# Kernel tuning notes

Measured on AMD Instinct MI355X. Metric: run time of the kernel, lower is better.

The kernel has to match this reference:

```python
import jax, jax.numpy as jnp
import numpy as np

B, S, D, H = 4, 2048, 1024, 16
DK = D // H
NEG = -1e9  # stand-in for -inf; keeps softmax grads NaN-free, same math after softmax


def setup_inputs() -> dict:
    key = jax.random.key(0)
    ks = jax.random.split(key, 8)
    scale = 0.02
    return {
        "q": jax.random.normal(ks[0], (B, S, D), jnp.float32),
        "k": jax.random.normal(ks[1], (B, S, D), jnp.float32),
        "v": jax.random.normal(ks[2], (B, S, D), jnp.float32),
        "mask": jnp.ones((B, S), jnp.int32),
        "Wq": jax.random.normal(ks[3], (D, D), jnp.float32) * scale,
        "bq": jnp.zeros((D,), jnp.float32),
        "Wk": jax.random.normal(ks[4], (D, D), jnp.float32) * scale,
        "bk": jnp.zeros((D,), jnp.float32),
        "Wv": jax.random.normal(ks[5], (D, D), jnp.float32) * scale,
        "bv": jnp.zeros((D,), jnp.float32),
        "Wp": jax.random.normal(ks[6], (D, D), jnp.float32) * scale,
        "bp": jnp.zeros((D,), jnp.float32),
    }


def reference(q, k, v, mask, Wq, bq, Wk, bk, Wv, bv, Wp, bp):
    # torch.nn.Linear: y = x @ W.T + b
    Q = q @ Wq.T + bq  # [B,S,D]
    K = k @ Wk.T + bk
    V = v @ Wv.T + bv
    # split heads -> [B,H,S,dk]
    Q = Q.reshape(B, S, H, DK).transpose(0, 2, 1, 3)
    K = K.reshape(B, S, H, DK).transpose(0, 2, 1, 3)
    V = V.reshape(B, S, H, DK).transpose(0, 2, 1, 3)
    Sc = jnp.einsum("bhqd,bhkd->bhqk", Q, K) / jnp.sqrt(jnp.float32(DK))
    # padding mask: [B,1,1,Sk]
    Sc = jnp.where(mask[:, None, None, :] == 0, NEG, Sc)
    # causal mask (tril), as in the registered buffer
    causal = jnp.tril(jnp.ones((S, S), jnp.bool_))
    Sc = jnp.where(causal, Sc, NEG)
    A = jax.nn.softmax(Sc, axis=-1)  # attn_drop with p=0 is identity
    x = jnp.einsum("bhqk,bhkd->bhqd", A, V)
    x = x.transpose(0, 2, 1, 3).reshape(B, S, D)
    return x @ Wp.T + bp
```

## Files before the change

### kernel.cpp

```cpp
#include <hip/hip_runtime.h>
#include <stdint.h>


#define SZB (8192u * 1024u * 2u)
#define WSZ (1024u * 1024u * 2u)

typedef __attribute__((ext_vector_type(8))) short  short8;
typedef __attribute__((ext_vector_type(4))) float  f32x4;

#define MFMA16(a, b, c) __builtin_amdgcn_mfma_f32_16x16x32_bf16(a, b, c, 0, 0, 0)

__device__ __forceinline__ ushort f2bf(float f) {
  uint32_t u = __float_as_uint(f);
  u += 0x7FFF + ((u >> 16) & 1);
  return (ushort)(u >> 16);
}
__device__ __forceinline__ short8 cvt8(float4 a, float4 b) {
  short8 r;
  r[0] = (short)f2bf(a.x); r[1] = (short)f2bf(a.y);
  r[2] = (short)f2bf(a.z); r[3] = (short)f2bf(a.w);
  r[4] = (short)f2bf(b.x); r[5] = (short)f2bf(b.y);
  r[6] = (short)f2bf(b.z); r[7] = (short)f2bf(b.w);
  return r;
}
__device__ __forceinline__ void gl_lds16(const ushort* g, ushort* l) {
  __builtin_amdgcn_global_load_lds(
      (__attribute__((address_space(1))) void*)g,
      (__attribute__((address_space(3))) void*)l, 16, 0, 0);
}

__global__ __launch_bounds__(256) void cvt_w(
    const float* __restrict__ Wq, const float* __restrict__ Wk,
    const float* __restrict__ Wv, const float* __restrict__ Wp,
    ushort* __restrict__ Wqb, ushort* __restrict__ Wkb,
    ushort* __restrict__ Wvb, ushort* __restrict__ Wpb) {
  const int z = blockIdx.y;
  const float* s = (z == 0) ? Wq : (z == 1) ? Wk : (z == 2) ? Wv : Wp;
  ushort* d = (z == 0) ? Wqb : (z == 1) ? Wkb : (z == 2) ? Wvb : Wpb;
  const size_t i = (size_t)(blockIdx.x * 256 + threadIdx.x) * 8;
  *(short8*)&d[i] = cvt8(*(const float4*)&s[i], *(const float4*)&s[i + 4]);
}

__global__ __launch_bounds__(256) void cvt_in(
    const float* __restrict__ q, const float* __restrict__ k,
    const float* __restrict__ v,
    ushort* __restrict__ qb2, ushort* __restrict__ kb2,
    ushort* __restrict__ vb2) {
  const int z = blockIdx.y;
  const float* s = (z == 0) ? q : (z == 1) ? k : v;
  ushort* d = (z == 0) ? qb2 : (z == 1) ? kb2 : vb2;
  const size_t i = (size_t)(blockIdx.x * 256 + threadIdx.x) * 8;
  *(short8*)&d[i] = cvt8(*(const float4*)&s[i], *(const float4*)&s[i + 4]);
}

__device__ __forceinline__ void gemm_core_mixed(
    const float* __restrict__ A, const ushort* __restrict__ Wb,
    ushort* As, ushort* Bs, int m0, int n0, f32x4 acc[4][4]) {
  const int tid  = threadIdx.x;
  const int w    = tid >> 6;
  const int lane = tid & 63;
  const int quad = lane >> 4;
  const int l16  = lane & 15;
  const int wm   = (w >> 1) * 64;
  const int wn   = (w & 1) * 64;
  const int r0   = tid >> 2;
  const int r1   = r0 + 64;
  const int c0   = (tid & 3) * 8;

  const ushort* Wg = Wb + (size_t)(n0 + w * 32 + (lane >> 2)) * 1024 + (lane & 3) * 8;
  const float*  Ag0 = A + (size_t)(m0 + r0) * 1024 + c0;
  const float*  Ag1 = A + (size_t)(m0 + r1) * 1024 + c0;

  float4 p0a = *(const float4*)(Ag0), p0b = *(const float4*)(Ag0 + 4);
  float4 p1a = *(const float4*)(Ag1), p1b = *(const float4*)(Ag1 + 4);

  for (int kt = 0; kt < 32; ++kt) {
    const int ko = kt * 32;
    __syncthreads();
    *(short8*)&As[r0 * 32 + c0] = cvt8(p0a, p0b);
    *(short8*)&As[r1 * 32 + c0] = cvt8(p1a, p1b);
    gl_lds16(Wg + ko,         &Bs[(w * 32) * 32]);
    gl_lds16(Wg + 16384 + ko, &Bs[(w * 32 + 16) * 32]);
    __syncthreads();
    if (kt < 31) {
      const int kn = ko + 32;
      p0a = *(const float4*)(Ag0 + kn); p0b = *(const float4*)(Ag0 + kn + 4);
      p1a = *(const float4*)(Ag1 + kn); p1b = *(const float4*)(Ag1 + kn + 4);
    }
    short8 af[4], bfr[4];
#pragma unroll
    for (int i = 0; i < 4; ++i)
      af[i] = *(const short8*)&As[(wm + i * 16 + l16) * 32 + quad * 8];
#pragma unroll
    for (int i = 0; i < 4; ++i)
      bfr[i] = *(const short8*)&Bs[(wn + i * 16 + l16) * 32 + quad * 8];
#pragma unroll
    for (int i = 0; i < 4; ++i)
#pragma unroll
      for (int j = 0; j < 4; ++j)
        acc[i][j] = MFMA16(af[i], bfr[j], acc[i][j]);
  }
}

__device__ __forceinline__ void gemm_core_bf(
    const ushort* __restrict__ A, const ushort* __restrict__ Wb,
    ushort* As, ushort* Bs, int m0, int n0, f32x4 acc[4][4]) {
  const int tid  = threadIdx.x;
  const int w    = tid >> 6;
  const int lane = tid & 63;
  const int quad = lane >> 4;
  const int l16  = lane & 15;
  const int wm   = (w >> 1) * 64;
  const int wn   = (w & 1) * 64;

  const ushort* Ag = A + (size_t)(m0 + w * 32 + (lane >> 2)) * 1024 + (lane & 3) * 8;
  const ushort* Wg = Wb + (size_t)(n0 + w * 32 + (lane >> 2)) * 1024 + (lane & 3) * 8;

  for (int kt = 0; kt < 32; ++kt) {
    const int ko = kt * 32;
    gl_lds16(Ag + ko,         &As[(w * 32) * 32]);
    gl_lds16(Ag + 16384 + ko, &As[(w * 32 + 16) * 32]);
    gl_lds16(Wg + ko,         &Bs[(w * 32) * 32]);
    gl_lds16(Wg + 16384 + ko, &Bs[(w * 32 + 16) * 32]);
    __syncthreads();

    short8 af[4], bfr[4];
#pragma unroll
    for (int i = 0; i < 4; ++i)
      af[i] = *(const short8*)&As[(wm + i * 16 + l16) * 32 + quad * 8];
#pragma unroll
    for (int i = 0; i < 4; ++i)
      bfr[i] = *(const short8*)&Bs[(wn + i * 16 + l16) * 32 + quad * 8];
#pragma unroll
    for (int i = 0; i < 4; ++i)
#pragma unroll
      for (int j = 0; j < 4; ++j)
        acc[i][j] = MFMA16(af[i], bfr[j], acc[i][j]);
    __syncthreads();
  }
}

__global__ __launch_bounds__(256) void gemm_qkv(
    const ushort* __restrict__ qb2, const ushort* __restrict__ kb2,
    const ushort* __restrict__ vb2, const float* __restrict__ vin, int v_bf,
    const ushort* __restrict__ Wqb, const ushort* __restrict__ Wkb, const ushort* __restrict__ Wvb,
    const float* __restrict__ bq, const float* __restrict__ bk, const float* __restrict__ bv,
    ushort* __restrict__ Qb, ushort* __restrict__ Kb, ushort* __restrict__ Vt) {
  __shared__ ushort As[128 * 32];
  __shared__ ushort Bs[128 * 32];

  const int z = blockIdx.z;
  const ushort* W    = (z == 0) ? Wqb : (z == 1) ? Wkb : Wvb;
  const float*  bias = (z == 0) ? bq  : (z == 1) ? bk  : bv;

  const int m0 = blockIdx.x * 128;
  const int n0 = blockIdx.y * 128;

  f32x4 acc[4][4] = {};
  if (z == 2 && !v_bf) {
    gemm_core_mixed(vin, W, As, Bs, m0, n0, acc);
  } else {
    const ushort* A = (z == 0) ? qb2 : (z == 1) ? kb2 : vb2;
    gemm_core_bf(A, W, As, Bs, m0, n0, acc);
  }

  const int tid  = threadIdx.x;
  const int w    = tid >> 6;
  const int lane = tid & 63;
  const int quad = lane >> 4;
  const int l16  = lane & 15;
  const int wm   = (w >> 1) * 64;
  const int wn   = (w & 1) * 64;

  float bvv[4];
#pragma unroll
  for (int j = 0; j < 4; ++j) bvv[j] = bias[n0 + wn + j * 16 + l16];

  if (z < 2) {
    ushort* Out = (z == 0) ? Qb : Kb;
    const float sc = (z == 0) ? 0.1803368801f : 1.0f;
#pragma unroll
    for (int i = 0; i < 4; ++i) {
      const int m = m0 + wm + i * 16 + quad * 4;
#pragma unroll
      for (int j = 0; j < 4; ++j) {
        const int n = n0 + wn + j * 16 + l16;
#pragma unroll
        for (int r = 0; r < 4; ++r)
          Out[(size_t)(m + r) * 1024 + n] = f2bf((acc[i][j][r] + bvv[j]) * sc);
      }
    }
  } else {
#pragma unroll
    for (int i = 0; i < 4; ++i) {
      const int mrow = m0 + wm + i * 16 + quad * 4;
      const int bb   = mrow >> 11;
      const int s0   = mrow & 2047;
#pragma unroll
      for (int j = 0; j < 4; ++j) {
        const int n = n0 + wn + j * 16 + l16;
        ushort4 pk;
        pk.x = f2bf(acc[i][j][0] + bvv[j]);
        pk.y = f2bf(acc[i][j][1] + bvv[j]);
        pk.z = f2bf(acc[i][j][2] + bvv[j]);
        pk.w = f2bf(acc[i][j][3] + bvv[j]);
        *(ushort4*)&Vt[(size_t)((bb * 16 + (n >> 6)) * 64 + (n & 63)) * 2048 + s0] = pk;
      }
    }
  }
}

__global__ __launch_bounds__(256, 4) void attn(
    ushort* __restrict__ Qb, const ushort* __restrict__ Kb,
    const ushort* __restrict__ Vt, const int* __restrict__ mask) {
  __shared__ ushort Ks[64 * 68];
  __shared__ ushort Vts[64 * 68];
  __shared__ ushort Ps[4][16 * 68];

  const int bh = blockIdx.y;
  const int b = bh >> 4, h = bh & 15;
  const int tid = threadIdx.x, w = tid >> 6, lane = tid & 63;
  const int quad = lane >> 4, l16 = lane & 15;

  short8 kst[2], vst[2];
  int pmn[4];

  auto ld_tile = [&](int k0) {
#pragma unroll
    for (int i = 0; i < 2; ++i) {
      const int c = tid + 256 * i;
      kst[i] = *(const short8*)&Kb[(size_t)(b * 2048 + k0 + (c >> 3)) * 1024 +
                                   h * 64 + (c & 7) * 8];
      vst[i] = *(const short8*)&Vt[(size_t)(bh * 64 + (c >> 3)) * 2048 +
                                   k0 + (c & 7) * 8];
    }
#pragma unroll
    for (int nj = 0; nj < 4; ++nj) pmn[nj] = mask[b * 2048 + k0 + nj * 16 + l16];
  };

#pragma unroll 1
  for (int seg = 0; seg < 2; ++seg) {
    const int qt = seg ? (31 - (int)blockIdx.x) : (int)blockIdx.x;
    const int q0 = qt * 64;

    const size_t qoff = (size_t)(b * 2048 + q0 + w * 16 + l16) * 1024 + h * 64 + quad * 8;
    const short8 qf0 = *(const short8*)&Qb[qoff];
    const short8 qf1 = *(const short8*)&Qb[qoff + 32];

    f32x4 oacc[4] = {};
    float lsum[4] = {0.f, 0.f, 0.f, 0.f};

    ld_tile(0);

    for (int kt = 0; kt <= qt; ++kt) {
      __syncthreads();
#pragma unroll
      for (int i = 0; i < 2; ++i) {
        const int c = tid + 256 * i;
        *(short8*)&Ks[(c >> 3) * 68 + (c & 7) * 8]  = kst[i];
        *(short8*)&Vts[(c >> 3) * 68 + (c & 7) * 8] = vst[i];
      }
      int pmc[4];
#pragma unroll
      for (int nj = 0; nj < 4; ++nj) pmc[nj] = pmn[nj];
      __syncthreads();

      if (kt < qt) ld_tile((kt + 1) * 64);

      f32x4 sc[4];
#pragma unroll
      for (int nj = 0; nj < 4; ++nj) {
        f32x4 z4 = {0.f, 0.f, 0.f, 0.f};
        const short8 kf0 = *(const short8*)&Ks[(nj * 16 + l16) * 68 + quad * 8];
        const short8 kf1 = *(const short8*)&Ks[(nj * 16 + l16) * 68 + 32 + quad * 8];
        z4 = MFMA16(qf0, kf0, z4);
        z4 = MFMA16(qf1, kf1, z4);
        sc[nj] = z4;
      }

      if (kt < qt) {
#pragma unroll
        for (int nj = 0; nj < 4; ++nj)
#pragma unroll
          for (int r = 0; r < 4; ++r) {
            const float e = (pmc[nj] != 0) ? sc[nj][r] : -1e5f;
            const float p = __builtin_amdgcn_exp2f(e);
            lsum[r] += p;
            Ps[w][(quad * 4 + r) * 68 + nj * 16 + l16] = f2bf(p);
          }
      } else {
        const int k0 = kt * 64;
#pragma unroll
        for (int nj = 0; nj < 4; ++nj) {
          const int key = k0 + nj * 16 + l16;
#pragma unroll
          for (int r = 0; r < 4; ++r) {
            const int qr = q0 + w * 16 + quad * 4 + r;
            const bool ok = (pmc[nj] != 0) && (key <= qr);
            const float e = ok ? sc[nj][r] : -1e5f;
            const float p = __builtin_amdgcn_exp2f(e);
            lsum[r] += p;
            Ps[w][(quad * 4 + r) * 68 + nj * 16 + l16] = f2bf(p);
          }
        }
      }

#pragma unroll
      for (int ks = 0; ks < 2; ++ks) {
        const short8 pf = *(const short8*)&Ps[w][l16 * 68 + ks * 32 + quad * 8];
#pragma unroll
        for (int nb = 0; nb < 4; ++nb) {
          const short8 vf = *(const short8*)&Vts[(nb * 16 + l16) * 68 + ks * 32 + quad * 8];
          oacc[nb] = MFMA16(pf, vf, oacc[nb]);
        }
      }
    }

#pragma unroll
    for (int r = 0; r < 4; ++r) {
      float v = lsum[r];
      v += __shfl_xor(v, 1);
      v += __shfl_xor(v, 2);
      v += __shfl_xor(v, 4);
      v += __shfl_xor(v, 8);
      lsum[r] = 1.0f / v;
    }
#pragma unroll
    for (int nb = 0; nb < 4; ++nb)
#pragma unroll
      for (int r = 0; r < 4; ++r) {
        const int q = q0 + w * 16 + quad * 4 + r;
        Qb[(size_t)(b * 2048 + q) * 1024 + h * 64 + nb * 16 + l16] =
            f2bf(oacc[nb][r] * lsum[r]);
      }
  }
}

__global__ __launch_bounds__(256) void gemm_proj(
    const ushort* __restrict__ Xin, const ushort* __restrict__ Wpb,
    const float* __restrict__ bp, float* __restrict__ Out) {
  __shared__ ushort As[128 * 32];
  __shared__ ushort Bs[128 * 32];

  const int m0 = blockIdx.x * 128;
  const int n0 = blockIdx.y * 128;

  f32x4 acc[4][4] = {};
  gemm_core_bf(Xin, Wpb, As, Bs, m0, n0, acc);

  const int tid  = threadIdx.x;
  const int w    = tid >> 6;
  const int lane = tid & 63;
  const int quad = lane >> 4;
  const int l16  = lane & 15;
  const int wm   = (w >> 1) * 64;
  const int wn   = (w & 1) * 64;

  float bvv[4];
#pragma unroll
  for (int j = 0; j < 4; ++j) bvv[j] = bp[n0 + wn + j * 16 + l16];

#pragma unroll
  for (int i = 0; i < 4; ++i) {
    const int m = m0 + wm + i * 16 + quad * 4;
#pragma unroll
    for (int j = 0; j < 4; ++j) {
      const int n = n0 + wn + j * 16 + l16;
#pragma unroll
      for (int r = 0; r < 4; ++r)
        Out[(size_t)(m + r) * 1024 + n] = acc[i][j][r] + bvv[j];
    }
  }
}

extern "C" void kernel_launch(void* const* d_in, const int* in_sizes, int n_in,
                              void* d_out, int out_size, void* d_ws, size_t ws_size,
                              hipStream_t stream) {
  const float* q    = (const float*)d_in[0];
  const float* k    = (const float*)d_in[1];
  const float* v    = (const float*)d_in[2];
  const int*   mask = (const int*)d_in[3];
  const float* Wq   = (const float*)d_in[4];
  const float* bq   = (const float*)d_in[5];
  const float* Wk   = (const float*)d_in[6];
  const float* bk   = (const float*)d_in[7];
  const float* Wv   = (const float*)d_in[8];
  const float* bv   = (const float*)d_in[9];
  const float* Wp   = (const float*)d_in[10];
  const float* bp   = (const float*)d_in[11];
  float* out = (float*)d_out;

  char* ws = (char*)d_ws;
  ushort* Qb  = (ushort*)(ws);
  ushort* Kb  = (ushort*)(ws + (size_t)SZB);
  ushort* Vt  = (ushort*)(ws + (size_t)2 * SZB);
  ushort* Wqb = (ushort*)(ws + (size_t)3 * SZB);
  ushort* Wkb = (ushort*)(ws + (size_t)3 * SZB + WSZ);
  ushort* Wvb = (ushort*)(ws + (size_t)3 * SZB + 2 * WSZ);
  ushort* Wpb = (ushort*)(ws + (size_t)3 * SZB + 3 * WSZ);

  ushort* qb2 = (ushort*)out;
  ushort* kb2 = (ushort*)((char*)out + (size_t)SZB);
  const size_t need_v = (size_t)3 * SZB + 4 * WSZ + SZB;
  const int v_bf = (ws_size >= need_v) ? 1 : 0;
  ushort* vb2 = v_bf ? (ushort*)(ws + (size_t)3 * SZB + 4 * WSZ) : nullptr;

  dim3 blk(256);
  cvt_w<<<dim3(512, 4), blk, 0, stream>>>(Wq, Wk, Wv, Wp, Wqb, Wkb, Wvb, Wpb);
  cvt_in<<<dim3(4096, 2 + v_bf), blk, 0, stream>>>(q, k, v, qb2, kb2, vb2);
  gemm_qkv<<<dim3(64, 8, 3), blk, 0, stream>>>(qb2, kb2, vb2, v, v_bf,
                                               Wqb, Wkb, Wvb, bq, bk, bv,
                                               Qb, Kb, Vt);
  attn<<<dim3(16, 64), blk, 0, stream>>>(Qb, Kb, Vt, mask);
  gemm_proj<<<dim3(64, 8), blk, 0, stream>>>(Qb, Wpb, bp, out);
}
```

Before: 352.4 us.

## Replace projection GEMM core with triple-buffered 512-thread swizzled-LDS pipeline

Rewrites the QKV and output projection GEMMs around a new core that uses 512-thread blocks with 256x128 tiles, a K-step of 64, and a three-slot LDS ring. Global-to-LDS loads are issued two stages ahead using vmcnt waits and a single barrier per step. Reads are XOR-swizzled to avoid bank conflicts, and MFMA issue priority is raised with setprio. The mixed fp32-input V path moves into a separate fallback kernel. The aim is to hide memory latency and cut sync overhead, at the cost of much more LDS per block (144 KB), which limits occupancy.

```diff
diff --git a/kernel.cpp b/kernel.cpp
--- a/kernel.cpp
+++ b/kernel.cpp
@@ -4,6 +4,8 @@
 
 #define SZB (8192u * 1024u * 2u)
 #define WSZ (1024u * 1024u * 2u)
+#define NKT 16
+#define SLOT 24576
 
 typedef __attribute__((ext_vector_type(8))) short  short8;
 typedef __attribute__((ext_vector_type(4))) float  f32x4;
@@ -53,9 +55,195 @@
   *(short8*)&d[i] = cvt8(*(const float4*)&s[i], *(const float4*)&s[i + 4]);
 }
 
-__device__ __forceinline__ void gemm_core_mixed(
-    const float* __restrict__ A, const ushort* __restrict__ Wb,
-    ushort* As, ushort* Bs, int m0, int n0, f32x4 acc[4][4]) {
+__device__ __forceinline__ void core8p(
+    const ushort* __restrict__ A, const ushort* __restrict__ Wb,
+    ushort* lds, int m0, int n0, f32x4 acc[4][4]) {
+  const int tid  = threadIdx.x;
+  const int w    = tid >> 6;
+  const int lane = tid & 63;
+  const int quad = lane >> 4;
+  const int l16  = lane & 15;
+  const int wm   = (w >> 1) * 64;
+  const int wn   = (w & 1) * 64;
+
+  const ushort* asrc[4];
+  const ushort* bsrc[2];
+#pragma unroll
+  for (int i = 0; i < 4; ++i) {
+    const int c = tid + 512 * i;
+    asrc[i] = A + (size_t)(m0 + (c >> 3)) * 1024 + ((c & 7) ^ ((c >> 3) & 7)) * 8;
+  }
+#pragma unroll
+  for (int i = 0; i < 2; ++i) {
+    const int c = tid + 512 * i;
+    bsrc[i] = Wb + (size_t)(n0 + (c >> 3)) * 1024 + ((c & 7) ^ ((c >> 3) & 7)) * 8;
+  }
+
+  auto stage = [&](int j, int s) {
+    ushort* base = lds + s * SLOT + w * 512;
+#pragma unroll
+    for (int i = 0; i < 4; ++i)
+      gl_lds16(asrc[i] + j * 64, base + i * 4096);
+#pragma unroll
+    for (int i = 0; i < 2; ++i)
+      gl_lds16(bsrc[i] + j * 64, base + 16384 + i * 4096);
+  };
+
+  const int rsw = (l16 & 7) * 8;
+  auto compute = [&](int s) {
+    const ushort* pA = lds + s * SLOT;
+    const ushort* pB = pA + 16384;
+    short8 a[4][2], b[4][2];
+#pragma unroll
+    for (int f = 0; f < 4; ++f)
+#pragma unroll
+      for (int ks = 0; ks < 2; ++ks) {
+        a[f][ks] = *(const short8*)&pA[(wm + f * 16 + l16) * 64 +
+                                       ((ks * 32 + quad * 8) ^ rsw)];
+        b[f][ks] = *(const short8*)&pB[(wn + f * 16 + l16) * 64 +
+                                       ((ks * 32 + quad * 8) ^ rsw)];
+      }
+    __builtin_amdgcn_s_setprio(1);
+#pragma unroll
+    for (int i = 0; i < 4; ++i)
+#pragma unroll
+      for (int j2 = 0; j2 < 4; ++j2) {
+        acc[i][j2] = MFMA16(a[i][0], b[j2][0], acc[i][j2]);
+        acc[i][j2] = MFMA16(a[i][1], b[j2][1], acc[i][j2]);
+      }
+    __builtin_amdgcn_s_setprio(0);
+  };
+
+  stage(0, 0);
+  stage(1, 1);
+  int s = 0;
+#pragma unroll 1
+  for (int j = 0; j < NKT - 1; ++j) {
+    asm volatile("s_waitcnt vmcnt(6)" ::: "memory");
+    __builtin_amdgcn_s_barrier();
+    __builtin_amdgcn_sched_barrier(0);
+    if (j < NKT - 2) {
+      int s2 = s + 2; if (s2 >= 3) s2 -= 3;
+      stage(j + 2, s2);
+    }
+    compute(s);
+    if (++s == 3) s = 0;
+  }
+  asm volatile("s_waitcnt vmcnt(0)" ::: "memory");
+  __builtin_amdgcn_s_barrier();
+  __builtin_amdgcn_sched_barrier(0);
+  compute(s);
+}
+
+__global__ __launch_bounds__(512, 2) void gemm_qkv8(
+    const ushort* __restrict__ qb2, const ushort* __restrict__ kb2,
+    const ushort* __restrict__ vb2,
+    const ushort* __restrict__ Wqb, const ushort* __restrict__ Wkb,
+    const ushort* __restrict__ Wvb,
+    const float* __restrict__ bq, const float* __restrict__ bk,
+    const float* __restrict__ bv,
+    ushort* __restrict__ Qb, ushort* __restrict__ Kb, ushort* __restrict__ Vt) {
+  __shared__ ushort lds[3 * SLOT];
+
+  const int z = blockIdx.z;
+  const ushort* A    = (z == 0) ? qb2 : (z == 1) ? kb2 : vb2;
+  const ushort* W    = (z == 0) ? Wqb : (z == 1) ? Wkb : Wvb;
+  const float*  bias = (z == 0) ? bq  : (z == 1) ? bk  : bv;
+
+  const int m0 = blockIdx.x * 256;
+  const int n0 = blockIdx.y * 128;
+
+  f32x4 acc[4][4] = {};
+  core8p(A, W, lds, m0, n0, acc);
+
+  const int tid  = threadIdx.x;
+  const int w    = tid >> 6;
+  const int lane = tid & 63;
+  const int quad = lane >> 4;
+  const int l16  = lane & 15;
+  const int wm   = (w >> 1) * 64;
+  const int wn   = (w & 1) * 64;
+
+  float bvv[4];
+#pragma unroll
+  for (int j = 0; j < 4; ++j) bvv[j] = bias[n0 + wn + j * 16 + l16];
+
+  if (z < 2) {
+    ushort* Out = (z == 0) ? Qb : Kb;
+    const float sc = (z == 0) ? 0.1803368801f : 1.0f;
+#pragma unroll
+    for (int i = 0; i < 4; ++i) {
+      const int m = m0 + wm + i * 16 + quad * 4;
+#pragma unroll
+      for (int j = 0; j < 4; ++j) {
+        const int n = n0 + wn + j * 16 + l16;
+#pragma unroll
+        for (int r = 0; r < 4; ++r)
+          Out[(size_t)(m + r) * 1024 + n] = f2bf((acc[i][j][r] + bvv[j]) * sc);
+      }
+    }
+  } else {
+#pragma unroll
+    for (int i = 0; i < 4; ++i) {
+      const int mrow = m0 + wm + i * 16 + quad * 4;
+      const int bb   = mrow >> 11;
+      const int s0   = mrow & 2047;
+#pragma unroll
+      for (int j = 0; j < 4; ++j) {
+        const int n = n0 + wn + j * 16 + l16;
+        ushort4 pk;
+        pk.x = f2bf(acc[i][j][0] + bvv[j]);
+        pk.y = f2bf(acc[i][j][1] + bvv[j]);
+        pk.z = f2bf(acc[i][j][2] + bvv[j]);
+        pk.w = f2bf(acc[i][j][3] + bvv[j]);
+        *(ushort4*)&Vt[(size_t)((bb * 16 + (n >> 6)) * 64 + (n & 63)) * 2048 + s0] = pk;
+      }
+    }
+  }
+}
+
+__global__ __launch_bounds__(512, 2) void gemm_proj8(
+    const ushort* __restrict__ Xin, const ushort* __restrict__ Wpb,
+    const float* __restrict__ bp, float* __restrict__ Out) {
+  __shared__ ushort lds[3 * SLOT];
+
+  const int m0 = blockIdx.x * 256;
+  const int n0 = blockIdx.y * 128;
+
+  f32x4 acc[4][4] = {};
+  core8p(Xin, Wpb, lds, m0, n0, acc);
+
+  const int tid  = threadIdx.x;
+  const int w    = tid >> 6;
+  const int lane = tid & 63;
+  const int quad = lane >> 4;
+  const int l16  = lane & 15;
+  const int wm   = (w >> 1) * 64;
+  const int wn   = (w & 1) * 64;
+
+  float bvv[4];
+#pragma unroll
+  for (int j = 0; j < 4; ++j) bvv[j] = bp[n0 + wn + j * 16 + l16];
+
+#pragma unroll
+  for (int i = 0; i < 4; ++i) {
+    const int m = m0 + wm + i * 16 + quad * 4;
+#pragma unroll
+    for (int j = 0; j < 4; ++j) {
+      const int n = n0 + wn + j * 16 + l16;
+#pragma unroll
+      for (int r = 0; r < 4; ++r)
+        Out[(size_t)(m + r) * 1024 + n] = acc[i][j][r] + bvv[j];
+    }
+  }
+}
+
+__global__ __launch_bounds__(256) void gemm_v_fb(
+    const float* __restrict__ vin, const ushort* __restrict__ Wvb,
+    const float* __restrict__ bv, ushort* __restrict__ Vt) {
+  __shared__ ushort As[128 * 32];
+  __shared__ ushort Bs[128 * 32];
+
   const int tid  = threadIdx.x;
   const int w    = tid >> 6;
   const int lane = tid & 63;
@@ -67,9 +255,13 @@
   const int r1   = r0 + 64;
   const int c0   = (tid & 3) * 8;
 
-  const ushort* Wg = Wb + (size_t)(n0 + w * 32 + (lane >> 2)) * 1024 + (lane & 3) * 8;
-  const float*  Ag0 = A + (size_t)(m0 + r0) * 1024 + c0;
-  const float*  Ag1 = A + (size_t)(m0 + r1) * 1024 + c0;
+  const int m0 = blockIdx.x * 128;
+  const int n0 = blockIdx.y * 128;
+
+  f32x4 acc[4][4] = {};
+  const ushort* Wg = Wvb + (size_t)(n0 + w * 32 + (lane >> 2)) * 1024 + (lane & 3) * 8;
+  const float*  Ag0 = vin + (size_t)(m0 + r0) * 1024 + c0;
+  const float*  Ag1 = vin + (size_t)(m0 + r1) * 1024 + c0;
 
   float4 p0a = *(const float4*)(Ag0), p0b = *(const float4*)(Ag0 + 4);
   float4 p1a = *(const float4*)(Ag1), p1b = *(const float4*)(Ag1 + 4);
@@ -100,112 +292,24 @@
       for (int j = 0; j < 4; ++j)
         acc[i][j] = MFMA16(af[i], bfr[j], acc[i][j]);
   }
-}
-
-__device__ __forceinline__ void gemm_core_bf(
-    const ushort* __restrict__ A, const ushort* __restrict__ Wb,
-    ushort* As, ushort* Bs, int m0, int n0, f32x4 acc[4][4]) {
-  const int tid  = threadIdx.x;
-  const int w    = tid >> 6;
-  const int lane = tid & 63;
-  const int quad = lane >> 4;
-  const int l16  = lane & 15;
-  const int wm   = (w >> 1) * 64;
-  const int wn   = (w & 1) * 64;
-
-  const ushort* Ag = A + (size_t)(m0 + w * 32 + (lane >> 2)) * 1024 + (lane & 3) * 8;
-  const ushort* Wg = Wb + (size_t)(n0 + w * 32 + (lane >> 2)) * 1024 + (lane & 3) * 8;
-
-  for (int kt = 0; kt < 32; ++kt) {
-    const int ko = kt * 32;
-    gl_lds16(Ag + ko,         &As[(w * 32) * 32]);
-    gl_lds16(Ag + 16384 + ko, &As[(w * 32 + 16) * 32]);
-    gl_lds16(Wg + ko,         &Bs[(w * 32) * 32]);
-    gl_lds16(Wg + 16384 + ko, &Bs[(w * 32 + 16) * 32]);
-    __syncthreads();
-
-    short8 af[4], bfr[4];
-#pragma unroll
-    for (int i = 0; i < 4; ++i)
-      af[i] = *(const short8*)&As[(wm + i * 16 + l16) * 32 + quad * 8];
-#pragma unroll
-    for (int i = 0; i < 4; ++i)
-      bfr[i] = *(const short8*)&Bs[(wn + i * 16 + l16) * 32 + quad * 8];
-#pragma unroll
-    for (int i = 0; i < 4; ++i)
-#pragma unroll
-      for (int j = 0; j < 4; ++j)
-        acc[i][j] = MFMA16(af[i], bfr[j], acc[i][j]);
-    __syncthreads();
-  }
-}
-
-__global__ __launch_bounds__(256) void gemm_qkv(
-    const ushort* __restrict__ qb2, const ushort* __restrict__ kb2,
-    const ushort* __restrict__ vb2, const float* __restrict__ vin, int v_bf,
-    const ushort* __restrict__ Wqb, const ushort* __restrict__ Wkb, const ushort* __restrict__ Wvb,
-    const float* __restrict__ bq, const float* __restrict__ bk, const float* __restrict__ bv,
-    ushort* __restrict__ Qb, ushort* __restrict__ Kb, ushort* __restrict__ Vt) {
-  __shared__ ushort As[128 * 32];
-  __shared__ ushort Bs[128 * 32];
-
-  const int z = blockIdx.z;
-  const ushort* W    = (z == 0) ? Wqb : (z == 1) ? Wkb : Wvb;
-  const float*  bias = (z == 0) ? bq  : (z == 1) ? bk  : bv;
-
-  const int m0 = blockIdx.x * 128;
-  const int n0 = blockIdx.y * 128;
-
-  f32x4 acc[4][4] = {};
-  if (z == 2 && !v_bf) {
-    gemm_core_mixed(vin, W, As, Bs, m0, n0, acc);
-  } else {
-    const ushort* A = (z == 0) ? qb2 : (z == 1) ? kb2 : vb2;
-    gemm_core_bf(A, W, As, Bs, m0, n0, acc);
-  }
-
-  const int tid  = threadIdx.x;
-  const int w    = tid >> 6;
-  const int lane = tid & 63;
-  const int quad = lane >> 4;
-  const int l16  = lane & 15;
-  const int wm   = (w >> 1) * 64;
-  const int wn   = (w & 1) * 64;
 
   float bvv[4];
 #pragma unroll
-  for (int j = 0; j < 4; ++j) bvv[j] = bias[n0 + wn + j * 16 + l16];
-
-  if (z < 2) {
-    ushort* Out = (z == 0) ? Qb : Kb;
-    const float sc = (z == 0) ? 0.1803368801f : 1.0f;
-#pragma unroll
-    for (int i = 0; i < 4; ++i) {
-      const int m = m0 + wm + i * 16 + quad * 4;
-#pragma unroll
-      for (int j = 0; j < 4; ++j) {
-        const int n = n0 + wn + j * 16 + l16;
-#pragma unroll
-        for (int r = 0; r < 4; ++r)
-          Out[(size_t)(m + r) * 1024 + n] = f2bf((acc[i][j][r] + bvv[j]) * sc);
-      }
-    }
-  } else {
-#pragma unroll
-    for (int i = 0; i < 4; ++i) {
-      const int mrow = m0 + wm + i * 16 + quad * 4;
-      const int bb   = mrow >> 11;
-      const int s0   = mrow & 2047;
-#pragma unroll
-      for (int j = 0; j < 4; ++j) {
-        const int n = n0 + wn + j * 16 + l16;
-        ushort4 pk;
-        pk.x = f2bf(acc[i][j][0] + bvv[j]);
-        pk.y = f2bf(acc[i][j][1] + bvv[j]);
-        pk.z = f2bf(acc[i][j][2] + bvv[j]);
-        pk.w = f2bf(acc[i][j][3] + bvv[j]);
-        *(ushort4*)&Vt[(size_t)((bb * 16 + (n >> 6)) * 64 + (n & 63)) * 2048 + s0] = pk;
-      }
+  for (int j = 0; j < 4; ++j) bvv[j] = bv[n0 + wn + j * 16 + l16];
+#pragma unroll
+  for (int i = 0; i < 4; ++i) {
+    const int mrow = m0 + wm + i * 16 + quad * 4;
+    const int bb   = mrow >> 11;
+    const int s0   = mrow & 2047;
+#pragma unroll
+    for (int j = 0; j < 4; ++j) {
+      const int n = n0 + wn + j * 16 + l16;
+      ushort4 pk;
+      pk.x = f2bf(acc[i][j][0] + bvv[j]);
+      pk.y = f2bf(acc[i][j][1] + bvv[j]);
+      pk.z = f2bf(acc[i][j][2] + bvv[j]);
+      pk.w = f2bf(acc[i][j][3] + bvv[j]);
+      *(ushort4*)&Vt[(size_t)((bb * 16 + (n >> 6)) * 64 + (n & 63)) * 2048 + s0] = pk;
     }
   }
 }
@@ -333,43 +437,6 @@
         Qb[(size_t)(b * 2048 + q) * 1024 + h * 64 + nb * 16 + l16] =
             f2bf(oacc[nb][r] * lsum[r]);
       }
-  }
-}
-
-__global__ __launch_bounds__(256) void gemm_proj(
-    const ushort* __restrict__ Xin, const ushort* __restrict__ Wpb,
-    const float* __restrict__ bp, float* __restrict__ Out) {
-  __shared__ ushort As[128 * 32];
-  __shared__ ushort Bs[128 * 32];
-
-  const int m0 = blockIdx.x * 128;
-  const int n0 = blockIdx.y * 128;
-
-  f32x4 acc[4][4] = {};
-  gemm_core_bf(Xin, Wpb, As, Bs, m0, n0, acc);
-
-  const int tid  = threadIdx.x;
-  const int w    = tid >> 6;
-  const int lane = tid & 63;
-  const int quad = lane >> 4;
-  const int l16  = lane & 15;
-  const int wm   = (w >> 1) * 64;
-  const int wn   = (w & 1) * 64;
-
-  float bvv[4];
-#pragma unroll
-  for (int j = 0; j < 4; ++j) bvv[j] = bp[n0 + wn + j * 16 + l16];
-
-#pragma unroll
-  for (int i = 0; i < 4; ++i) {
-    const int m = m0 + wm + i * 16 + quad * 4;
-#pragma unroll
-    for (int j = 0; j < 4; ++j) {
-      const int n = n0 + wn + j * 16 + l16;
-#pragma unroll
-      for (int r = 0; r < 4; ++r)
-        Out[(size_t)(m + r) * 1024 + n] = acc[i][j][r] + bvv[j];
-    }
   }
 }
 
@@ -405,12 +472,12 @@
   const int v_bf = (ws_size >= need_v) ? 1 : 0;
   ushort* vb2 = v_bf ? (ushort*)(ws + (size_t)3 * SZB + 4 * WSZ) : nullptr;
 
-  dim3 blk(256);
-  cvt_w<<<dim3(512, 4), blk, 0, stream>>>(Wq, Wk, Wv, Wp, Wqb, Wkb, Wvb, Wpb);
-  cvt_in<<<dim3(4096, 2 + v_bf), blk, 0, stream>>>(q, k, v, qb2, kb2, vb2);
-  gemm_qkv<<<dim3(64, 8, 3), blk, 0, stream>>>(qb2, kb2, vb2, v, v_bf,
-                                               Wqb, Wkb, Wvb, bq, bk, bv,
-                                               Qb, Kb, Vt);
-  attn<<<dim3(16, 64), blk, 0, stream>>>(Qb, Kb, Vt, mask);
-  gemm_proj<<<dim3(64, 8), blk, 0, stream>>>(Qb, Wpb, bp, out);
-}
+  cvt_w<<<dim3(512, 4), dim3(256), 0, stream>>>(Wq, Wk, Wv, Wp, Wqb, Wkb, Wvb, Wpb);
+  cvt_in<<<dim3(4096, 2 + v_bf), dim3(256), 0, stream>>>(q, k, v, qb2, kb2, vb2);
+  gemm_qkv8<<<dim3(32, 8, 2 + v_bf), dim3(512), 0, stream>>>(
+      qb2, kb2, vb2, Wqb, Wkb, Wvb, bq, bk, bv, Qb, Kb, Vt);
+  if (!v_bf)
+    gemm_v_fb<<<dim3(64, 8), dim3(256), 0, stream>>>(v, Wvb, bv, Vt);
+  attn<<<dim3(16, 64), dim3(256), 0, stream>>>(Qb, Kb, Vt, mask);
+  gemm_proj8<<<dim3(32, 8), dim3(512), 0, stream>>>(Qb, Wpb, bp, out);
+}
```

Measured after the change: 327.6 us. 1.08x faster.
